# Optimization experiments

Hardware: AMD Instinct MI355X
Metric: run time of the kernel (lower is better)

Reference implementation:

```python
import jax, jax.numpy as jnp
import numpy as np

LAYER_SIZES = [1024, 1024, 1024, 1024, 1024, 1024, 512]
MAX_PATHS = 128
BATCH = 128
N_LAYERS = len(LAYER_SIZES) - 1


def setup_inputs() -> dict:
    key = jax.random.key(0)
    keys = jax.random.split(key, 1 + 2 * N_LAYERS)
    inp = {"x": jax.random.normal(keys[0], (BATCH, LAYER_SIZES[0]), dtype=jnp.float32)}
    for i in range(N_LAYERS):
        inp[f"W{i}"] = jax.random.normal(keys[1 + 2 * i], (LAYER_SIZES[i], LAYER_SIZES[i + 1]), dtype=jnp.float32) * 0.01
        inp[f"b{i}"] = jax.random.normal(keys[2 + 2 * i], (LAYER_SIZES[i + 1],), dtype=jnp.float32) * 0.01
    return inp


def _layer(data, W, b):
    # data: [B, in_feat, P] -> [B, out_feat, 3P]
    B, _, P = data.shape
    O = W.shape[1]
    pos = jnp.einsum('bfp,fo->bpo', data, W) + b          # [B, P, O]; neg branch is exactly -pos
    branches = jnp.stack([-pos, jnp.zeros_like(pos), pos], axis=-1)  # [B, P, O, 3]
    # transpose(1,2) then reshape: interleave branches per source path, matching torch
    return branches.transpose(0, 2, 1, 3).reshape(B, O, P * 3)


def _prune(data, keep):
    # keep top-`keep` paths by L2 norm over the feature dim
    norms = jnp.linalg.norm(data, axis=1)                 # [B, P]
    _, idx = jax.lax.top_k(norms, keep)                   # [B, keep]
    return jnp.take_along_axis(data, idx[:, None, :], axis=-1)


def _forward(x, Ws, bs):
    data = x[:, :, None]                                   # [B, F, 1]
    for i in range(N_LAYERS):
        data = _layer(data, Ws[i], bs[i])
        if i < N_LAYERS - 1:
            data = jnp.tanh(data)
        if data.shape[-1] > MAX_PATHS:
            data = _prune(data, MAX_PATHS)
    # collapse with 'max_abs': per (batch, feature) pick path with largest |value|
    idx = jnp.argmax(jnp.abs(data), axis=-1, keepdims=True)
    output = jnp.take_along_axis(data, idx, axis=-1).squeeze(-1)
    return output, data


def reference(x, W0, b0, W1, b1, W2, b2, W3, b3, W4, b4, W5, b5):
    Ws = [W0, W1, W2, W3, W4, W5]
    bs = [b0, b1, b2, b3, b4, b5]
    return _forward(x, Ws, bs)
```

## Files before the change

kernel.cpp:

```cpp
#include <hip/hip_runtime.h>
#include <math.h>


using s8v = __attribute__((ext_vector_type(8))) short;
using f4v = __attribute__((ext_vector_type(4))) float;

__device__ __forceinline__ float bf2f(short b) {
  unsigned u = ((unsigned)(unsigned short)b) << 16;
  return __builtin_bit_cast(float, u);
}
__device__ __forceinline__ short f2bf(float f) {
  unsigned u = __builtin_bit_cast(unsigned, f);
  u = (u + 0x7FFFu + ((u >> 16) & 1u)) >> 16;
  return (short)u;
}

struct TWArgs {
  const float* W[6];
  short* Th[6];
  short* Tl[6];
  const float* x;
  short* A0h;
  short* A0l;
  float* zone;
};
__global__ void __launch_bounds__(256)
transW_all(TWArgs a) {
  const int z = blockIdx.z;
  const int t = threadIdx.x;
  if (z == 6) {
    int bid = blockIdx.y * 16 + blockIdx.x;
    if (bid < 128) {
      int i = (bid * 256 + t) * 4;
      float4 v = *(const float4*)&a.x[i];
      short4 h, l;
      h.x = f2bf(v.x); l.x = f2bf(v.x - bf2f(h.x));
      h.y = f2bf(v.y); l.y = f2bf(v.y - bf2f(h.y));
      h.z = f2bf(v.z); l.z = f2bf(v.z - bf2f(h.z));
      h.w = f2bf(v.w); l.w = f2bf(v.w - bf2f(h.w));
      *(short4*)&a.A0h[i] = h;
      *(short4*)&a.A0l[i] = l;
    } else if (bid < 176) {
      a.zone[(bid - 128) * 256 + t] = 0.f;
    }
    return;
  }
  const int N = (z == 5) ? 512 : 1024;
  const int n0 = blockIdx.x * 64, k0 = blockIdx.y * 64;
  if (n0 >= N) return;
  const float* __restrict__ W = a.W[z];
  short* __restrict__ Th = a.Th[z];
  short* __restrict__ Tl = a.Tl[z];
  __shared__ float tile[64][65];
  const int r = t >> 4, c4 = (t & 15) * 4;
#pragma unroll
  for (int i = 0; i < 4; ++i) {
    int rr = r + 16 * i;
    float4 v = *(const float4*)&W[(size_t)(k0 + rr) * N + n0 + c4];
    tile[rr][c4 + 0] = v.x;
    tile[rr][c4 + 1] = v.y;
    tile[rr][c4 + 2] = v.z;
    tile[rr][c4 + 3] = v.w;
  }
  __syncthreads();
#pragma unroll
  for (int i = 0; i < 4; ++i) {
    int n = r + 16 * i;
    short4 h, l;
    float f0 = tile[c4 + 0][n], f1 = tile[c4 + 1][n];
    float f2 = tile[c4 + 2][n], f3 = tile[c4 + 3][n];
    h.x = f2bf(f0); l.x = f2bf(f0 - bf2f(h.x));
    h.y = f2bf(f1); l.y = f2bf(f1 - bf2f(h.y));
    h.z = f2bf(f2); l.z = f2bf(f2 - bf2f(h.z));
    h.w = f2bf(f3); l.w = f2bf(f3 - bf2f(h.w));
    size_t o = (size_t)(n0 + n) * 1024 + k0 + c4;
    *(short4*)&Th[o] = h;
    *(short4*)&Tl[o] = l;
  }
}

template <int EPI, int D, int KS>
__global__ void __launch_bounds__(256, 3)
mfma_gemm(const short* __restrict__ Ah, const short* __restrict__ Al,
          const short* __restrict__ Bh, const short* __restrict__ Bl,
          const float* __restrict__ bias, short* __restrict__ Oh,
          short* __restrict__ Ol, float* __restrict__ Of,
          float* __restrict__ ns, float* __restrict__ dotv,
          float* __restrict__ nrmv, int N, int Dn) {
  constexpr int KC = 1024 / KS;
  constexpr int BKP = 40;
  __shared__ short As_h[64 * BKP], As_l[64 * BKP];
  __shared__ short Bs_h[64 * BKP], Bs_l[64 * BKP];
  __shared__ float et[64][68];
  const int t = threadIdx.x;
  const int row0 = blockIdx.y * 64;
  const int col0 = blockIdx.x * 64;
  const int kb = blockIdx.z * KC;
  const int sr = t >> 2, sko = (t & 3) * 8;
  const short* Ahp = Ah + (size_t)(row0 + sr) * 1024 + kb + sko;
  const short* Alp = Al + (size_t)(row0 + sr) * 1024 + kb + sko;
  const short* Bhp = Bh + (size_t)(col0 + sr) * 1024 + kb + sko;
  const short* Blp = Bl + (size_t)(col0 + sr) * 1024 + kb + sko;
  const int w = t >> 6, lane = t & 63;
  const int l16 = lane & 15, q = lane >> 4;
  const int wm0 = (w & 1) * 32, wn0 = (w >> 1) * 32;
  const int abase = (wm0 + l16) * BKP + q * 8;
  const int bbase = (wn0 + l16) * BKP + q * 8;
  f4v acc[2][2];
#pragma unroll
  for (int i = 0; i < 2; ++i)
#pragma unroll
    for (int j = 0; j < 2; ++j) acc[i][j] = (f4v){0.f, 0.f, 0.f, 0.f};
  uint4 rah = *(const uint4*)(Ahp);
  uint4 ral = *(const uint4*)(Alp);
  uint4 rbh = *(const uint4*)(Bhp);
  uint4 rbl = *(const uint4*)(Blp);
  for (int k0 = 0; k0 < KC; k0 += 32) {
    __syncthreads();
    *(uint4*)&As_h[sr * BKP + sko] = rah;
    *(uint4*)&As_l[sr * BKP + sko] = ral;
    *(uint4*)&Bs_h[sr * BKP + sko] = rbh;
    *(uint4*)&Bs_l[sr * BKP + sko] = rbl;
    if (k0 + 32 < KC) {
      rah = *(const uint4*)(Ahp + k0 + 32);
      ral = *(const uint4*)(Alp + k0 + 32);
      rbh = *(const uint4*)(Bhp + k0 + 32);
      rbl = *(const uint4*)(Blp + k0 + 32);
    }
    __syncthreads();
    s8v ah[2], al[2], bh[2], bl[2];
#pragma unroll
    for (int mt = 0; mt < 2; ++mt) {
      ah[mt] = *(const s8v*)&As_h[abase + mt * 16 * BKP];
      al[mt] = *(const s8v*)&As_l[abase + mt * 16 * BKP];
    }
#pragma unroll
    for (int nt = 0; nt < 2; ++nt) {
      bh[nt] = *(const s8v*)&Bs_h[bbase + nt * 16 * BKP];
      bl[nt] = *(const s8v*)&Bs_l[bbase + nt * 16 * BKP];
    }
#pragma unroll
    for (int mt = 0; mt < 2; ++mt)
#pragma unroll
      for (int nt = 0; nt < 2; ++nt) {
        acc[mt][nt] = __builtin_amdgcn_mfma_f32_16x16x32_bf16(
            ah[mt], bh[nt], acc[mt][nt], 0, 0, 0);
        acc[mt][nt] = __builtin_amdgcn_mfma_f32_16x16x32_bf16(
            ah[mt], bl[nt], acc[mt][nt], 0, 0, 0);
        acc[mt][nt] = __builtin_amdgcn_mfma_f32_16x16x32_bf16(
            al[mt], bh[nt], acc[mt][nt], 0, 0, 0);
      }
  }

#pragma unroll
  for (int mt = 0; mt < 2; ++mt)
#pragma unroll
    for (int nt = 0; nt < 2; ++nt)
#pragma unroll
      for (int r = 0; r < 4; ++r)
        et[wm0 + mt * 16 + q * 4 + r][wn0 + nt * 16 + l16] = acc[mt][nt][r];
  __syncthreads();
  const int rl = t >> 2, cc = (t & 3) * 16;
  float v[16];
#pragma unroll
  for (int j = 0; j < 16; ++j) v[j] = et[rl][cc + j];
  const int rr = row0 + rl;

  if constexpr (EPI == 0) {
    const int R = (int)gridDim.y << 6;
    float* dst = Of + ((size_t)blockIdx.z * R + rr) * N + col0 + cc;
#pragma unroll
    for (int i = 0; i < 4; ++i)
      *(float4*)&dst[4 * i] =
          make_float4(v[4 * i], v[4 * i + 1], v[4 * i + 2], v[4 * i + 3]);
  } else if constexpr (EPI == 1) {
    const int b = rr / D, u = rr - b * D;
    const size_t ob = (size_t)(b * Dn) * (size_t)N + col0 + cc;
    const size_t om = ob + (size_t)(1 + 2 * u) * N;
    const size_t op = ob + (size_t)(2 + 2 * u) * N;
    uint mh[8], ml[8], ph[8], pl[8];
    float sm = 0.f, sp = 0.f;
#pragma unroll
    for (int j2 = 0; j2 < 8; ++j2) {
      float bc0 = bias[col0 + cc + 2 * j2];
      float bc1 = bias[col0 + cc + 2 * j2 + 1];
      float tm0 = tanhf(bc0 - v[2 * j2]), tm1 = tanhf(bc1 - v[2 * j2 + 1]);
      float tp0 = tanhf(bc0 + v[2 * j2]), tp1 = tanhf(bc1 + v[2 * j2 + 1]);
      short h0 = f2bf(tm0), h1 = f2bf(tm1);
      short g0 = f2bf(tm0 - bf2f(h0)), g1 = f2bf(tm1 - bf2f(h1));
      mh[j2] = (uint)(unsigned short)h0 | ((uint)(unsigned short)h1 << 16);
      ml[j2] = (uint)(unsigned short)g0 | ((uint)(unsigned short)g1 << 16);
      h0 = f2bf(tp0); h1 = f2bf(tp1);
      g0 = f2bf(tp0 - bf2f(h0)); g1 = f2bf(tp1 - bf2f(h1));
      ph[j2] = (uint)(unsigned short)h0 | ((uint)(unsigned short)h1 << 16);
      pl[j2] = (uint)(unsigned short)g0 | ((uint)(unsigned short)g1 << 16);
      sm = fmaf(tm0, tm0, fmaf(tm1, tm1, sm));
      sp = fmaf(tp0, tp0, fmaf(tp1, tp1, sp));
    }
    *(uint4*)&Oh[om] = make_uint4(mh[0], mh[1], mh[2], mh[3]);
    *(uint4*)&Oh[om + 8] = make_uint4(mh[4], mh[5], mh[6], mh[7]);
    *(uint4*)&Ol[om] = make_uint4(ml[0], ml[1], ml[2], ml[3]);
    *(uint4*)&Ol[om + 8] = make_uint4(ml[4], ml[5], ml[6], ml[7]);
    *(uint4*)&Oh[op] = make_uint4(ph[0], ph[1], ph[2], ph[3]);
    *(uint4*)&Oh[op + 8] = make_uint4(ph[4], ph[5], ph[6], ph[7]);
    *(uint4*)&Ol[op] = make_uint4(pl[0], pl[1], pl[2], pl[3]);
    *(uint4*)&Ol[op + 8] = make_uint4(pl[4], pl[5], pl[6], pl[7]);
    sm += __shfl_xor(sm, 1); sm += __shfl_xor(sm, 2);
    sp += __shfl_xor(sp, 1); sp += __shfl_xor(sp, 2);
    if ((t & 3) == 0) {
      atomicAdd(&ns[b * Dn + 1 + 2 * u], sm);
      atomicAdd(&ns[b * Dn + 2 + 2 * u], sp);
    }
    if (u == 0) {
      uint zh[8], zl[8];
      float sz = 0.f;
#pragma unroll
      for (int j2 = 0; j2 < 8; ++j2) {
        float tz0 = tanhf(bias[col0 + cc + 2 * j2]);
        float tz1 = tanhf(bias[col0 + cc + 2 * j2 + 1]);
        short h0 = f2bf(tz0), h1 = f2bf(tz1);
        short g0 = f2bf(tz0 - bf2f(h0)), g1 = f2bf(tz1 - bf2f(h1));
        zh[j2] = (uint)(unsigned short)h0 | ((uint)(unsigned short)h1 << 16);
        zl[j2] = (uint)(unsigned short)g0 | ((uint)(unsigned short)g1 << 16);
        sz = fmaf(tz0, tz0, fmaf(tz1, tz1, sz));
      }
      *(uint4*)&Oh[ob] = make_uint4(zh[0], zh[1], zh[2], zh[3]);
      *(uint4*)&Oh[ob + 8] = make_uint4(zh[4], zh[5], zh[6], zh[7]);
      *(uint4*)&Ol[ob] = make_uint4(zl[0], zl[1], zl[2], zl[3]);
      *(uint4*)&Ol[ob + 8] = make_uint4(zl[4], zl[5], zl[6], zl[7]);
      sz += __shfl_xor(sz, 1); sz += __shfl_xor(sz, 2);
      if ((t & 3) == 0) atomicAdd(&ns[b * Dn], sz);
    }
  } else {
    float nr = 0.f, dt = 0.f;
    float* dst = Of + (size_t)rr * N + col0 + cc;
#pragma unroll
    for (int j = 0; j < 16; ++j) {
      nr = fmaf(v[j], v[j], nr);
      dt = fmaf(v[j], bias[col0 + cc + j], dt);
    }
#pragma unroll
    for (int i = 0; i < 4; ++i)
      *(float4*)&dst[4 * i] =
          make_float4(v[4 * i], v[4 * i + 1], v[4 * i + 2], v[4 * i + 3]);
    nr += __shfl_xor(nr, 1); nr += __shfl_xor(nr, 2);
    dt += __shfl_xor(dt, 1); dt += __shfl_xor(dt, 2);
    if ((t & 3) == 0) {
      atomicAdd(&nrmv[rr], nr);
      atomicAdd(&dotv[rr], dt);
    }
  }
}

template <int KS>
__global__ void __launch_bounds__(256)
comb0_hl(const float* __restrict__ P, const float* __restrict__ bias,
         short* __restrict__ Oh, short* __restrict__ Ol, int R, int N) {
  int i = blockIdx.x * 256 + threadIdx.x;
  int n4 = N >> 2;
  int r = i / n4, c4 = (i - r * n4) * 4;
  float4 y = *(const float4*)&P[(size_t)r * N + c4];
  size_t stride = (size_t)R * N;
#pragma unroll
  for (int ks = 1; ks < KS; ++ks) {
    const float4 p = *(const float4*)&P[ks * stride + (size_t)r * N + c4];
    y.x += p.x; y.y += p.y; y.z += p.z; y.w += p.w;
  }
  float4 bc = *(const float4*)(bias + c4);
  float t0 = tanhf(bc.x + y.x), t1 = tanhf(bc.y + y.y);
  float t2 = tanhf(bc.z + y.z), t3 = tanhf(bc.w + y.w);
  short4 h, l;
  h.x = f2bf(t0); l.x = f2bf(t0 - bf2f(h.x));
  h.y = f2bf(t1); l.y = f2bf(t1 - bf2f(h.y));
  h.z = f2bf(t2); l.z = f2bf(t2 - bf2f(h.z));
  h.w = f2bf(t3); l.w = f2bf(t3 - bf2f(h.w));
  *(short4*)&Oh[(size_t)r * N + c4] = h;
  *(short4*)&Ol[(size_t)r * N + c4] = l;
}

template <int KS, int D>
__global__ void __launch_bounds__(256)
comb1_hl(const float* __restrict__ P, const float* __restrict__ bias,
         short* __restrict__ Oh, short* __restrict__ Ol, int R, int N,
         int Dn) {
  int i = blockIdx.x * 256 + threadIdx.x;
  int n4 = N >> 2;
  int r = i / n4, c4 = (i - r * n4) * 4;
  int b = r / D, u = r - b * D;
  float4 y = *(const float4*)&P[(size_t)r * N + c4];
  size_t stride = (size_t)R * N;
#pragma unroll
  for (int ks = 1; ks < KS; ++ks) {
    const float4 p = *(const float4*)&P[ks * stride + (size_t)r * N + c4];
    y.x += p.x; y.y += p.y; y.z += p.z; y.w += p.w;
  }
  float4 bc = *(const float4*)(bias + c4);
  size_t ob = (size_t)(b * Dn) * N + c4;
  size_t om = ob + (size_t)(1 + 2 * u) * N;
  size_t op = ob + (size_t)(2 + 2 * u) * N;
  {
    float t0 = tanhf(bc.x - y.x), t1 = tanhf(bc.y - y.y);
    float t2 = tanhf(bc.z - y.z), t3 = tanhf(bc.w - y.w);
    short4 h, l;
    h.x = f2bf(t0); l.x = f2bf(t0 - bf2f(h.x));
    h.y = f2bf(t1); l.y = f2bf(t1 - bf2f(h.y));
    h.z = f2bf(t2); l.z = f2bf(t2 - bf2f(h.z));
    h.w = f2bf(t3); l.w = f2bf(t3 - bf2f(h.w));
    *(short4*)&Oh[om] = h;
    *(short4*)&Ol[om] = l;
  }
  {
    float t0 = tanhf(bc.x + y.x), t1 = tanhf(bc.y + y.y);
    float t2 = tanhf(bc.z + y.z), t3 = tanhf(bc.w + y.w);
    short4 h, l;
    h.x = f2bf(t0); l.x = f2bf(t0 - bf2f(h.x));
    h.y = f2bf(t1); l.y = f2bf(t1 - bf2f(h.y));
    h.z = f2bf(t2); l.z = f2bf(t2 - bf2f(h.z));
    h.w = f2bf(t3); l.w = f2bf(t3 - bf2f(h.w));
    *(short4*)&Oh[op] = h;
    *(short4*)&Ol[op] = l;
  }
  if (u == 0) {
    float t0 = tanhf(bc.x), t1 = tanhf(bc.y);
    float t2 = tanhf(bc.z), t3 = tanhf(bc.w);
    short4 h, l;
    h.x = f2bf(t0); l.x = f2bf(t0 - bf2f(h.x));
    h.y = f2bf(t1); l.y = f2bf(t1 - bf2f(h.y));
    h.z = f2bf(t2); l.z = f2bf(t2 - bf2f(h.z));
    h.w = f2bf(t3); l.w = f2bf(t3 - bf2f(h.w));
    *(short4*)&Oh[ob] = h;
    *(short4*)&Ol[ob] = l;
  }
}

__global__ void __launch_bounds__(256)
prune4_k(const float* __restrict__ ns, int* __restrict__ kept4) {
  int b = blockIdx.x, t = threadIdx.x;
  __shared__ float nss[31];
  __shared__ float key[243];
  __shared__ int cls[243];
  if (t < 31) nss[t] = ns[b * 31 + t];
  __syncthreads();
  if (t < 243) {
    int j = t / 3, t4 = t - 3 * j;
    int d0 = j / 27, d1 = (j / 9) % 3, d2 = (j / 3) % 3, d3 = j % 3;
    int u = 0;
    u = (d0 == 1) ? 0 : (1 + 2 * u + (d0 == 2));
    u = (d1 == 1) ? 0 : (1 + 2 * u + (d1 == 2));
    u = (d2 == 1) ? 0 : (1 + 2 * u + (d2 == 2));
    u = (d3 == 1) ? 0 : (1 + 2 * u + (d3 == 2));
    cls[t] = u;
    key[t] = (t4 == 1) ? 0.f : nss[u];
  }
  __syncthreads();
  if (t < 243) {
    float k = key[t];
    int rank = 0;
    for (int e = 0; e < 243; ++e) {
      float ke = key[e];
      rank += (ke > k) || (ke == k && e < t);
    }
    if (rank < 128) {
      int t4 = t - 3 * (t / 3);
      kept4[b * 128 + rank] = (cls[t] << 1) | (t4 == 2 ? 1 : 0);
    }
  }
}

__global__ void __launch_bounds__(384)
prune5_k(const float* __restrict__ dotv, const float* __restrict__ nrmv,
         const float* __restrict__ b5, const int* __restrict__ kept4,
         int* __restrict__ kept5) {
  int b = blockIdx.x, t = threadIdx.x;
  __shared__ float red[384];
  __shared__ float pns[128];
  __shared__ float key[384];
  float p = 0.f;
  for (int o = t; o < 512; o += 384) p = fmaf(b5[o], b5[o], p);
  red[t] = p;
  __syncthreads();
  if (t < 128) red[t] = red[t] + red[t + 128] + red[t + 256];
  __syncthreads();
  if (t < 64) red[t] += red[t + 64];
  __syncthreads();
  if (t < 32) red[t] += red[t + 32];
  __syncthreads();
  if (t < 16) red[t] += red[t + 16];
  __syncthreads();
  if (t < 8) red[t] += red[t + 8];
  __syncthreads();
  if (t < 4) red[t] += red[t + 4];
  __syncthreads();
  if (t < 2) red[t] += red[t + 2];
  __syncthreads();
  if (t == 0) red[0] += red[1];
  __syncthreads();
  float nb5 = red[0];
  if (t < 128) {
    int k4 = kept4[b * 128 + t];
    int c = k4 >> 1;
    float s = (k4 & 1) ? 1.f : -1.f;
    pns[t] = nb5 + nrmv[b * 31 + c] + s * 2.f * dotv[b * 31 + c];
  }
  __syncthreads();
  int m = t / 3, tt = t - 3 * m;
  key[t] = (tt == 1) ? 0.f : pns[m];
  __syncthreads();
  float k = key[t];
  int rank = 0;
  for (int e = 0; e < 384; ++e) {
    float ke = key[e];
    rank += (ke > k) || (ke == k && e < t);
  }
  if (rank < 128) kept5[b * 128 + rank] = (m << 1) | (tt == 2 ? 1 : 0);
}

__global__ void __launch_bounds__(256)
finalize_k(const float* __restrict__ Y5, const float* __restrict__ b5,
           const int* __restrict__ kept4, const int* __restrict__ kept5,
           float* __restrict__ out, float* __restrict__ dataout) {
  const int b = blockIdx.y;
  const int o0 = blockIdx.x * 64;
  __shared__ float Ys[31][65];
  __shared__ float bias_s[64];
  __shared__ float vt[64][130];
  __shared__ float ra[64][4];
  __shared__ float rv[64][4];
  const int t = threadIdx.x;
  for (int idx = t; idx < 31 * 64; idx += 256) {
    int c = idx >> 6, o = idx & 63;
    Ys[c][o] = Y5[((size_t)b * 31 + c) * 512 + o0 + o];
  }
  if (t < 64) bias_s[t] = b5[o0 + t];
  const int rr = t & 127, oh = t >> 7;
  int k5 = kept5[b * 128 + rr];
  int m = k5 >> 1;
  float sig = (k5 & 1) ? 1.f : -1.f;
  int k4 = kept4[b * 128 + m];
  int cc = k4 >> 1;
  float s4 = (k4 & 1) ? 1.f : -1.f;
  float afac = sig * s4;
  __syncthreads();
#pragma unroll
  for (int ol = 0; ol < 32; ++ol) {
    int o = oh * 32 + ol;
    float v = sig * bias_s[o] + afac * Ys[cc][o];
    dataout[((size_t)b * 512 + o0 + o) * 128 + rr] = v;
    vt[o][rr] = v;
  }
  __syncthreads();
  int o = t >> 2, q = t & 3;
  float bestv = vt[o][q * 32];
  float besta = fabsf(bestv);
  for (int i = 1; i < 32; ++i) {
    float v = vt[o][q * 32 + i];
    float a = fabsf(v);
    if (a > besta) {
      besta = a;
      bestv = v;
    }
  }
  ra[o][q] = besta;
  rv[o][q] = bestv;
  __syncthreads();
  if (t < 64) {
    float ba = ra[t][0], bv = rv[t][0];
#pragma unroll
    for (int qq = 1; qq < 4; ++qq) {
      if (ra[t][qq] > ba) {
        ba = ra[t][qq];
        bv = rv[t][qq];
      }
    }
    out[(size_t)b * 512 + o0 + t] = bv;
  }
}

extern "C" void kernel_launch(void* const* d_in, const int* in_sizes, int n_in,
                              void* d_out, int out_size, void* d_ws,
                              size_t ws_size, hipStream_t stream) {
  const float* x = (const float*)d_in[0];
  const float* Wt[6];
  const float* bs[6];
  for (int i = 0; i < 6; ++i) {
    Wt[i] = (const float*)d_in[1 + 2 * i];
    bs[i] = (const float*)d_in[2 + 2 * i];
  }
  char* base = (char*)d_ws;
  short* A0h = (short*)(base + 0);
  short* A0l = (short*)(base + 262144);
  short* Wh[6], *Wl[6];
  {
    size_t off = 524288;
    for (int i = 0; i < 6; ++i) {
      size_t sz = (i < 5) ? 2097152 : 1048576;
      Wh[i] = (short*)(base + off);
      Wl[i] = (short*)(base + off + sz);
      off += 2 * sz;
    }
  }
  short* C1h = (short*)(base + 23592960), *C1l = (short*)(base + 23855104);
  short* C2h = (short*)(base + 24117248), *C2l = (short*)(base + 24903680);
  short* C3h = (short*)(base + 25690112), *C3l = (short*)(base + 27525120);
  short* C4h = (short*)(base + 29360128), *C4l = (short*)(base + 33292288);
  short* C5h = (short*)(base + 524288);
  short* C5l = (short*)(base + 8912896);
  float* PA = (float*)(base + 29360128);
  float* PB = (float*)(base + 524288);
  float* Y5 = (float*)(base + 23592960);
  float* ns = (float*)(base + 37224448);
  float* dotv = ns + 3968;
  float* nrmv = dotv + 3968;
  int* kept4 = (int*)(base + 37273600);
  int* kept5 = (int*)(base + 37339136);
  float* outp = (float*)d_out;
  float* dataout = outp + 128 * 512;

  dim3 blk(256);
  TWArgs twa;
  for (int i = 0; i < 6; ++i) {
    twa.W[i] = Wt[i];
    twa.Th[i] = Wh[i];
    twa.Tl[i] = Wl[i];
  }
  twa.x = x;
  twa.A0h = A0h;
  twa.A0l = A0l;
  twa.zone = ns;
  transW_all<<<dim3(16, 16, 7), blk, 0, stream>>>(twa);

  mfma_gemm<0, 1, 8><<<dim3(16, 2, 8), blk, 0, stream>>>(
      A0h, A0l, Wh[0], Wl[0], nullptr, nullptr, nullptr, PA, nullptr, nullptr,
      nullptr, 1024, 1);
  comb0_hl<8><<<dim3(128), blk, 0, stream>>>(PA, bs[0], C1h, C1l, 128, 1024);
  mfma_gemm<0, 1, 8><<<dim3(16, 2, 8), blk, 0, stream>>>(
      C1h, C1l, Wh[1], Wl[1], nullptr, nullptr, nullptr, PA, nullptr, nullptr,
      nullptr, 1024, 3);
  comb1_hl<8, 1><<<dim3(128), blk, 0, stream>>>(PA, bs[1], C2h, C2l, 128, 1024,
                                                3);
  mfma_gemm<0, 3, 4><<<dim3(16, 6, 4), blk, 0, stream>>>(
      C2h, C2l, Wh[2], Wl[2], nullptr, nullptr, nullptr, PA, nullptr, nullptr,
      nullptr, 1024, 7);
  comb1_hl<4, 3><<<dim3(384), blk, 0, stream>>>(PA, bs[2], C3h, C3l, 384, 1024,
                                                7);
  mfma_gemm<0, 7, 2><<<dim3(16, 14, 2), blk, 0, stream>>>(
      C3h, C3l, Wh[3], Wl[3], nullptr, nullptr, nullptr, PB, nullptr, nullptr,
      nullptr, 1024, 15);
  comb1_hl<2, 7><<<dim3(896), blk, 0, stream>>>(PB, bs[3], C4h, C4l, 896, 1024,
                                                15);
  mfma_gemm<1, 15, 1><<<dim3(16, 30), blk, 0, stream>>>(
      C4h, C4l, Wh[4], Wl[4], bs[4], C5h, C5l, nullptr, ns, nullptr, nullptr,
      1024, 31);
  prune4_k<<<dim3(128), blk, 0, stream>>>(ns, kept4);
  mfma_gemm<2, 31, 1><<<dim3(8, 62), blk, 0, stream>>>(
      C5h, C5l, Wh[5], Wl[5], bs[5], nullptr, nullptr, Y5, nullptr, dotv, nrmv,
      512, 0);
  prune5_k<<<dim3(128), dim3(384), 0, stream>>>(dotv, nrmv, bs[5], kept4,
                                                kept5);
  finalize_k<<<dim3(8, 128), blk, 0, stream>>>(Y5, bs[5], kept4, kept5, outp,
                                               dataout);
}
```

Measured before the change: 242.5 us.

## Add 128x128-tile GEMM variant for the three largest layers

Splits the GEMM into a small-tile variant (64x64, store only) for the early layers and a new 128x128-tile variant with 4x4 MFMA fragments per wave for layers 3-5. The big tile doubles register and LDS reuse of the A/B fragments, stages bias in shared memory, and reuses the tile LDS for a two-pass epilogue. The layer-3 split-K factor changes from 2 to 4. Workspace buffers are relocated so the bigger outputs no longer alias the weight buffers. The trade-off is fewer blocks per layer (e.g. 120 and 124 for layers 4 and 5), lower occupancy (launch bound 2), and higher register pressure.

After: 393.5 us. 62.3% more time.

```diff
diff --git a/kernel.cpp b/kernel.cpp
--- a/kernel.cpp
+++ b/kernel.cpp
@@ -79,14 +79,11 @@
   }
 }
 
-template <int EPI, int D, int KS>
+template <int KS>
 __global__ void __launch_bounds__(256, 3)
-mfma_gemm(const short* __restrict__ Ah, const short* __restrict__ Al,
-          const short* __restrict__ Bh, const short* __restrict__ Bl,
-          const float* __restrict__ bias, short* __restrict__ Oh,
-          short* __restrict__ Ol, float* __restrict__ Of,
-          float* __restrict__ ns, float* __restrict__ dotv,
-          float* __restrict__ nrmv, int N, int Dn) {
+mfma_gemm_s(const short* __restrict__ Ah, const short* __restrict__ Al,
+            const short* __restrict__ Bh, const short* __restrict__ Bl,
+            float* __restrict__ Of, int N) {
   constexpr int KC = 1024 / KS;
   constexpr int BKP = 40;
   __shared__ short As_h[64 * BKP], As_l[64 * BKP];
@@ -151,7 +148,6 @@
             al[mt], bh[nt], acc[mt][nt], 0, 0, 0);
       }
   }
-
 #pragma unroll
   for (int mt = 0; mt < 2; ++mt)
 #pragma unroll
@@ -165,89 +161,211 @@
 #pragma unroll
   for (int j = 0; j < 16; ++j) v[j] = et[rl][cc + j];
   const int rr = row0 + rl;
-
-  if constexpr (EPI == 0) {
-    const int R = (int)gridDim.y << 6;
-    float* dst = Of + ((size_t)blockIdx.z * R + rr) * N + col0 + cc;
-#pragma unroll
-    for (int i = 0; i < 4; ++i)
-      *(float4*)&dst[4 * i] =
-          make_float4(v[4 * i], v[4 * i + 1], v[4 * i + 2], v[4 * i + 3]);
-  } else if constexpr (EPI == 1) {
-    const int b = rr / D, u = rr - b * D;
-    const size_t ob = (size_t)(b * Dn) * (size_t)N + col0 + cc;
-    const size_t om = ob + (size_t)(1 + 2 * u) * N;
-    const size_t op = ob + (size_t)(2 + 2 * u) * N;
-    uint mh[8], ml[8], ph[8], pl[8];
-    float sm = 0.f, sp = 0.f;
-#pragma unroll
-    for (int j2 = 0; j2 < 8; ++j2) {
-      float bc0 = bias[col0 + cc + 2 * j2];
-      float bc1 = bias[col0 + cc + 2 * j2 + 1];
-      float tm0 = tanhf(bc0 - v[2 * j2]), tm1 = tanhf(bc1 - v[2 * j2 + 1]);
-      float tp0 = tanhf(bc0 + v[2 * j2]), tp1 = tanhf(bc1 + v[2 * j2 + 1]);
-      short h0 = f2bf(tm0), h1 = f2bf(tm1);
-      short g0 = f2bf(tm0 - bf2f(h0)), g1 = f2bf(tm1 - bf2f(h1));
-      mh[j2] = (uint)(unsigned short)h0 | ((uint)(unsigned short)h1 << 16);
-      ml[j2] = (uint)(unsigned short)g0 | ((uint)(unsigned short)g1 << 16);
-      h0 = f2bf(tp0); h1 = f2bf(tp1);
-      g0 = f2bf(tp0 - bf2f(h0)); g1 = f2bf(tp1 - bf2f(h1));
-      ph[j2] = (uint)(unsigned short)h0 | ((uint)(unsigned short)h1 << 16);
-      pl[j2] = (uint)(unsigned short)g0 | ((uint)(unsigned short)g1 << 16);
-      sm = fmaf(tm0, tm0, fmaf(tm1, tm1, sm));
-      sp = fmaf(tp0, tp0, fmaf(tp1, tp1, sp));
-    }
-    *(uint4*)&Oh[om] = make_uint4(mh[0], mh[1], mh[2], mh[3]);
-    *(uint4*)&Oh[om + 8] = make_uint4(mh[4], mh[5], mh[6], mh[7]);
-    *(uint4*)&Ol[om] = make_uint4(ml[0], ml[1], ml[2], ml[3]);
-    *(uint4*)&Ol[om + 8] = make_uint4(ml[4], ml[5], ml[6], ml[7]);
-    *(uint4*)&Oh[op] = make_uint4(ph[0], ph[1], ph[2], ph[3]);
-    *(uint4*)&Oh[op + 8] = make_uint4(ph[4], ph[5], ph[6], ph[7]);
-    *(uint4*)&Ol[op] = make_uint4(pl[0], pl[1], pl[2], pl[3]);
-    *(uint4*)&Ol[op + 8] = make_uint4(pl[4], pl[5], pl[6], pl[7]);
-    sm += __shfl_xor(sm, 1); sm += __shfl_xor(sm, 2);
-    sp += __shfl_xor(sp, 1); sp += __shfl_xor(sp, 2);
-    if ((t & 3) == 0) {
-      atomicAdd(&ns[b * Dn + 1 + 2 * u], sm);
-      atomicAdd(&ns[b * Dn + 2 + 2 * u], sp);
-    }
-    if (u == 0) {
-      uint zh[8], zl[8];
-      float sz = 0.f;
-#pragma unroll
-      for (int j2 = 0; j2 < 8; ++j2) {
-        float tz0 = tanhf(bias[col0 + cc + 2 * j2]);
-        float tz1 = tanhf(bias[col0 + cc + 2 * j2 + 1]);
-        short h0 = f2bf(tz0), h1 = f2bf(tz1);
-        short g0 = f2bf(tz0 - bf2f(h0)), g1 = f2bf(tz1 - bf2f(h1));
-        zh[j2] = (uint)(unsigned short)h0 | ((uint)(unsigned short)h1 << 16);
-        zl[j2] = (uint)(unsigned short)g0 | ((uint)(unsigned short)g1 << 16);
-        sz = fmaf(tz0, tz0, fmaf(tz1, tz1, sz));
-      }
-      *(uint4*)&Oh[ob] = make_uint4(zh[0], zh[1], zh[2], zh[3]);
-      *(uint4*)&Oh[ob + 8] = make_uint4(zh[4], zh[5], zh[6], zh[7]);
-      *(uint4*)&Ol[ob] = make_uint4(zl[0], zl[1], zl[2], zl[3]);
-      *(uint4*)&Ol[ob + 8] = make_uint4(zl[4], zl[5], zl[6], zl[7]);
-      sz += __shfl_xor(sz, 1); sz += __shfl_xor(sz, 2);
-      if ((t & 3) == 0) atomicAdd(&ns[b * Dn], sz);
-    }
-  } else {
-    float nr = 0.f, dt = 0.f;
-    float* dst = Of + (size_t)rr * N + col0 + cc;
-#pragma unroll
-    for (int j = 0; j < 16; ++j) {
-      nr = fmaf(v[j], v[j], nr);
-      dt = fmaf(v[j], bias[col0 + cc + j], dt);
-    }
-#pragma unroll
-    for (int i = 0; i < 4; ++i)
-      *(float4*)&dst[4 * i] =
-          make_float4(v[4 * i], v[4 * i + 1], v[4 * i + 2], v[4 * i + 3]);
-    nr += __shfl_xor(nr, 1); nr += __shfl_xor(nr, 2);
-    dt += __shfl_xor(dt, 1); dt += __shfl_xor(dt, 2);
-    if ((t & 3) == 0) {
-      atomicAdd(&nrmv[rr], nr);
-      atomicAdd(&dotv[rr], dt);
+  const int R = (int)gridDim.y << 6;
+  float* dst = Of + ((size_t)blockIdx.z * R + rr) * N + col0 + cc;
+#pragma unroll
+  for (int i = 0; i < 4; ++i)
+    *(float4*)&dst[4 * i] =
+        make_float4(v[4 * i], v[4 * i + 1], v[4 * i + 2], v[4 * i + 3]);
+}
+
+template <int EPI, int D, int KS>
+__global__ void __launch_bounds__(256, 2)
+mfma_gemm_b(const short* __restrict__ Ah, const short* __restrict__ Al,
+            const short* __restrict__ Bh, const short* __restrict__ Bl,
+            const float* __restrict__ bias, short* __restrict__ Oh,
+            short* __restrict__ Ol, float* __restrict__ Of,
+            float* __restrict__ ns, float* __restrict__ dotv,
+            float* __restrict__ nrmv, int N, int Dn) {
+  constexpr int KC = 1024 / KS;
+  constexpr int BKP = 40;
+  __shared__ short smem[4 * 128 * BKP];
+  short* As_h = smem;
+  short* As_l = smem + 128 * BKP;
+  short* Bs_h = smem + 2 * 128 * BKP;
+  short* Bs_l = smem + 3 * 128 * BKP;
+  float* et = (float*)smem;
+  __shared__ float bias_s[128];
+  const int t = threadIdx.x;
+  const int row0 = blockIdx.y * 128;
+  const int col0 = blockIdx.x * 128;
+  const int kb = blockIdx.z * KC;
+  if (EPI >= 1 && t < 32)
+    *(float4*)&bias_s[t * 4] = *(const float4*)&bias[col0 + t * 4];
+  const int sr = t >> 1, sko = (t & 1) * 16;
+  const short* Ahp = Ah + (size_t)(row0 + sr) * 1024 + kb + sko;
+  const short* Alp = Al + (size_t)(row0 + sr) * 1024 + kb + sko;
+  const short* Bhp = Bh + (size_t)(col0 + sr) * 1024 + kb + sko;
+  const short* Blp = Bl + (size_t)(col0 + sr) * 1024 + kb + sko;
+  const int w = t >> 6, lane = t & 63;
+  const int l16 = lane & 15, q = lane >> 4;
+  const int wm0 = (w & 1) * 64, wn0 = (w >> 1) * 64;
+  f4v acc[4][4];
+#pragma unroll
+  for (int i = 0; i < 4; ++i)
+#pragma unroll
+    for (int j = 0; j < 4; ++j) acc[i][j] = (f4v){0.f, 0.f, 0.f, 0.f};
+  uint4 rah[2], ral[2], rbh[2], rbl[2];
+#pragma unroll
+  for (int j = 0; j < 2; ++j) {
+    rah[j] = *(const uint4*)(Ahp + 8 * j);
+    ral[j] = *(const uint4*)(Alp + 8 * j);
+    rbh[j] = *(const uint4*)(Bhp + 8 * j);
+    rbl[j] = *(const uint4*)(Blp + 8 * j);
+  }
+  for (int k0 = 0; k0 < KC; k0 += 32) {
+    __syncthreads();
+#pragma unroll
+    for (int j = 0; j < 2; ++j) {
+      *(uint4*)&As_h[sr * BKP + sko + 8 * j] = rah[j];
+      *(uint4*)&As_l[sr * BKP + sko + 8 * j] = ral[j];
+      *(uint4*)&Bs_h[sr * BKP + sko + 8 * j] = rbh[j];
+      *(uint4*)&Bs_l[sr * BKP + sko + 8 * j] = rbl[j];
+    }
+    if (k0 + 32 < KC) {
+#pragma unroll
+      for (int j = 0; j < 2; ++j) {
+        rah[j] = *(const uint4*)(Ahp + k0 + 32 + 8 * j);
+        ral[j] = *(const uint4*)(Alp + k0 + 32 + 8 * j);
+        rbh[j] = *(const uint4*)(Bhp + k0 + 32 + 8 * j);
+        rbl[j] = *(const uint4*)(Blp + k0 + 32 + 8 * j);
+      }
+    }
+    __syncthreads();
+    s8v ah[4], al[4], bh[4], bl[4];
+#pragma unroll
+    for (int mt = 0; mt < 4; ++mt) {
+      int o = (wm0 + mt * 16 + l16) * BKP + q * 8;
+      ah[mt] = *(const s8v*)&As_h[o];
+      al[mt] = *(const s8v*)&As_l[o];
+    }
+#pragma unroll
+    for (int nt = 0; nt < 4; ++nt) {
+      int o = (wn0 + nt * 16 + l16) * BKP + q * 8;
+      bh[nt] = *(const s8v*)&Bs_h[o];
+      bl[nt] = *(const s8v*)&Bs_l[o];
+    }
+#pragma unroll
+    for (int mt = 0; mt < 4; ++mt)
+#pragma unroll
+      for (int nt = 0; nt < 4; ++nt) {
+        acc[mt][nt] = __builtin_amdgcn_mfma_f32_16x16x32_bf16(
+            ah[mt], bh[nt], acc[mt][nt], 0, 0, 0);
+        acc[mt][nt] = __builtin_amdgcn_mfma_f32_16x16x32_bf16(
+            ah[mt], bl[nt], acc[mt][nt], 0, 0, 0);
+        acc[mt][nt] = __builtin_amdgcn_mfma_f32_16x16x32_bf16(
+            al[mt], bh[nt], acc[mt][nt], 0, 0, 0);
+      }
+  }
+
+  const int rl = t >> 2, cc4 = (t & 3) * 32;
+  for (int pp = 0; pp < 2; ++pp) {
+    __syncthreads();
+    if ((w & 1) == pp) {
+#pragma unroll
+      for (int mt = 0; mt < 4; ++mt)
+#pragma unroll
+        for (int nt = 0; nt < 4; ++nt)
+#pragma unroll
+          for (int r = 0; r < 4; ++r)
+            et[(mt * 16 + q * 4 + r) * 132 + wn0 + nt * 16 + l16] =
+                acc[mt][nt][r];
+    }
+    __syncthreads();
+    float v[32];
+#pragma unroll
+    for (int j = 0; j < 32; ++j) v[j] = et[rl * 132 + cc4 + j];
+    const int rr = row0 + pp * 64 + rl;
+
+    if constexpr (EPI == 0) {
+      const int R = (int)gridDim.y << 7;
+      float* dst = Of + ((size_t)blockIdx.z * R + rr) * N + col0 + cc4;
+#pragma unroll
+      for (int i = 0; i < 8; ++i)
+        *(float4*)&dst[4 * i] =
+            make_float4(v[4 * i], v[4 * i + 1], v[4 * i + 2], v[4 * i + 3]);
+    } else if constexpr (EPI == 1) {
+      const int b = rr / D, u = rr - b * D;
+      const size_t ob = (size_t)(b * Dn) * (size_t)N + col0 + cc4;
+      const size_t om = ob + (size_t)(1 + 2 * u) * N;
+      const size_t op = ob + (size_t)(2 + 2 * u) * N;
+      uint mh[16], ml[16], qh[16], ql[16];
+      float sm = 0.f, sp = 0.f;
+#pragma unroll
+      for (int j2 = 0; j2 < 16; ++j2) {
+        float bc0 = bias_s[cc4 + 2 * j2];
+        float bc1 = bias_s[cc4 + 2 * j2 + 1];
+        float tm0 = tanhf(bc0 - v[2 * j2]), tm1 = tanhf(bc1 - v[2 * j2 + 1]);
+        float tp0 = tanhf(bc0 + v[2 * j2]), tp1 = tanhf(bc1 + v[2 * j2 + 1]);
+        short h0 = f2bf(tm0), h1 = f2bf(tm1);
+        short g0 = f2bf(tm0 - bf2f(h0)), g1 = f2bf(tm1 - bf2f(h1));
+        mh[j2] = (uint)(unsigned short)h0 | ((uint)(unsigned short)h1 << 16);
+        ml[j2] = (uint)(unsigned short)g0 | ((uint)(unsigned short)g1 << 16);
+        h0 = f2bf(tp0); h1 = f2bf(tp1);
+        g0 = f2bf(tp0 - bf2f(h0)); g1 = f2bf(tp1 - bf2f(h1));
+        qh[j2] = (uint)(unsigned short)h0 | ((uint)(unsigned short)h1 << 16);
+        ql[j2] = (uint)(unsigned short)g0 | ((uint)(unsigned short)g1 << 16);
+        sm = fmaf(tm0, tm0, fmaf(tm1, tm1, sm));
+        sp = fmaf(tp0, tp0, fmaf(tp1, tp1, sp));
+      }
+#pragma unroll
+      for (int i = 0; i < 4; ++i) {
+        *(uint4*)&Oh[om + 8 * i] =
+            make_uint4(mh[4 * i], mh[4 * i + 1], mh[4 * i + 2], mh[4 * i + 3]);
+        *(uint4*)&Ol[om + 8 * i] =
+            make_uint4(ml[4 * i], ml[4 * i + 1], ml[4 * i + 2], ml[4 * i + 3]);
+        *(uint4*)&Oh[op + 8 * i] =
+            make_uint4(qh[4 * i], qh[4 * i + 1], qh[4 * i + 2], qh[4 * i + 3]);
+        *(uint4*)&Ol[op + 8 * i] =
+            make_uint4(ql[4 * i], ql[4 * i + 1], ql[4 * i + 2], ql[4 * i + 3]);
+      }
+      sm += __shfl_xor(sm, 1); sm += __shfl_xor(sm, 2);
+      sp += __shfl_xor(sp, 1); sp += __shfl_xor(sp, 2);
+      if ((t & 3) == 0) {
+        atomicAdd(&ns[b * Dn + 1 + 2 * u], sm);
+        atomicAdd(&ns[b * Dn + 2 + 2 * u], sp);
+      }
+      if (u == 0) {
+        float sz = 0.f;
+        uint zh[16], zl[16];
+#pragma unroll
+        for (int j2 = 0; j2 < 16; ++j2) {
+          float tz0 = tanhf(bias_s[cc4 + 2 * j2]);
+          float tz1 = tanhf(bias_s[cc4 + 2 * j2 + 1]);
+          short h0 = f2bf(tz0), h1 = f2bf(tz1);
+          short g0 = f2bf(tz0 - bf2f(h0)), g1 = f2bf(tz1 - bf2f(h1));
+          zh[j2] = (uint)(unsigned short)h0 | ((uint)(unsigned short)h1 << 16);
+          zl[j2] = (uint)(unsigned short)g0 | ((uint)(unsigned short)g1 << 16);
+          sz = fmaf(tz0, tz0, fmaf(tz1, tz1, sz));
+        }
+#pragma unroll
+        for (int i = 0; i < 4; ++i) {
+          *(uint4*)&Oh[ob + 8 * i] = make_uint4(zh[4 * i], zh[4 * i + 1],
+                                                zh[4 * i + 2], zh[4 * i + 3]);
+          *(uint4*)&Ol[ob + 8 * i] = make_uint4(zl[4 * i], zl[4 * i + 1],
+                                                zl[4 * i + 2], zl[4 * i + 3]);
+        }
+        sz += __shfl_xor(sz, 1); sz += __shfl_xor(sz, 2);
+        if ((t & 3) == 0) atomicAdd(&ns[b * Dn], sz);
+      }
+    } else {
+      float nr = 0.f, dt = 0.f;
+      float* dst = Of + (size_t)rr * N + col0 + cc4;
+#pragma unroll
+      for (int j = 0; j < 32; ++j) {
+        nr = fmaf(v[j], v[j], nr);
+        dt = fmaf(v[j], bias_s[cc4 + j], dt);
+      }
+#pragma unroll
+      for (int i = 0; i < 8; ++i)
+        *(float4*)&dst[4 * i] =
+            make_float4(v[4 * i], v[4 * i + 1], v[4 * i + 2], v[4 * i + 3]);
+      nr += __shfl_xor(nr, 1); nr += __shfl_xor(nr, 2);
+      dt += __shfl_xor(dt, 1); dt += __shfl_xor(dt, 2);
+      if ((t & 3) == 0) {
+        atomicAdd(&nrmv[rr], nr);
+        atomicAdd(&dotv[rr], dt);
+      }
     }
   }
 }
@@ -503,16 +621,16 @@
   short* C2h = (short*)(base + 24117248), *C2l = (short*)(base + 24903680);
   short* C3h = (short*)(base + 25690112), *C3l = (short*)(base + 27525120);
   short* C4h = (short*)(base + 29360128), *C4l = (short*)(base + 33292288);
-  short* C5h = (short*)(base + 524288);
-  short* C5l = (short*)(base + 8912896);
-  float* PA = (float*)(base + 29360128);
-  float* PB = (float*)(base + 524288);
-  float* Y5 = (float*)(base + 23592960);
-  float* ns = (float*)(base + 37224448);
+  short* C5h = (short*)(base + 37224448);
+  short* C5l = (short*)(base + 45350912);
+  float* Y5 = (float*)(base + 53477376);
+  float* PA = (float*)(base + 61603840);
+  float* PB = (float*)(base + 67895296);
+  float* ns = (float*)(base + 82575360);
   float* dotv = ns + 3968;
   float* nrmv = dotv + 3968;
-  int* kept4 = (int*)(base + 37273600);
-  int* kept5 = (int*)(base + 37339136);
+  int* kept4 = (int*)(base + 82624512);
+  int* kept5 = (int*)(base + 82690048);
   float* outp = (float*)d_out;
   float* dataout = outp + 128 * 512;
 
@@ -529,30 +647,27 @@
   twa.zone = ns;
   transW_all<<<dim3(16, 16, 7), blk, 0, stream>>>(twa);
 
-  mfma_gemm<0, 1, 8><<<dim3(16, 2, 8), blk, 0, stream>>>(
-      A0h, A0l, Wh[0], Wl[0], nullptr, nullptr, nullptr, PA, nullptr, nullptr,
-      nullptr, 1024, 1);
+  mfma_gemm_s<8><<<dim3(16, 2, 8), blk, 0, stream>>>(A0h, A0l, Wh[0], Wl[0],
+                                                     PA, 1024);
   comb0_hl<8><<<dim3(128), blk, 0, stream>>>(PA, bs[0], C1h, C1l, 128, 1024);
-  mfma_gemm<0, 1, 8><<<dim3(16, 2, 8), blk, 0, stream>>>(
-      C1h, C1l, Wh[1], Wl[1], nullptr, nullptr, nullptr, PA, nullptr, nullptr,
-      nullptr, 1024, 3);
+  mfma_gemm_s<8><<<dim3(16, 2, 8), blk, 0, stream>>>(C1h, C1l, Wh[1], Wl[1],
+                                                     PA, 1024);
   comb1_hl<8, 1><<<dim3(128), blk, 0, stream>>>(PA, bs[1], C2h, C2l, 128, 1024,
                                                 3);
-  mfma_gemm<0, 3, 4><<<dim3(16, 6, 4), blk, 0, stream>>>(
-      C2h, C2l, Wh[2], Wl[2], nullptr, nullptr, nullptr, PA, nullptr, nullptr,
-      nullptr, 1024, 7);
+  mfma_gemm_s<4><<<dim3(16, 6, 4), blk, 0, stream>>>(C2h, C2l, Wh[2], Wl[2],
+                                                     PA, 1024);
   comb1_hl<4, 3><<<dim3(384), blk, 0, stream>>>(PA, bs[2], C3h, C3l, 384, 1024,
                                                 7);
-  mfma_gemm<0, 7, 2><<<dim3(16, 14, 2), blk, 0, stream>>>(
+  mfma_gemm_b<0, 7, 4><<<dim3(8, 7, 4), blk, 0, stream>>>(
       C3h, C3l, Wh[3], Wl[3], nullptr, nullptr, nullptr, PB, nullptr, nullptr,
       nullptr, 1024, 15);
-  comb1_hl<2, 7><<<dim3(896), blk, 0, stream>>>(PB, bs[3], C4h, C4l, 896, 1024,
+  comb1_hl<4, 7><<<dim3(896), blk, 0, stream>>>(PB, bs[3], C4h, C4l, 896, 1024,
                                                 15);
-  mfma_gemm<1, 15, 1><<<dim3(16, 30), blk, 0, stream>>>(
+  mfma_gemm_b<1, 15, 1><<<dim3(8, 15), blk, 0, stream>>>(
       C4h, C4l, Wh[4], Wl[4], bs[4], C5h, C5l, nullptr, ns, nullptr, nullptr,
       1024, 31);
   prune4_k<<<dim3(128), blk, 0, stream>>>(ns, kept4);
-  mfma_gemm<2, 31, 1><<<dim3(8, 62), blk, 0, stream>>>(
+  mfma_gemm_b<2, 31, 1><<<dim3(4, 31), blk, 0, stream>>>(
       C5h, C5l, Wh[5], Wl[5], bs[5], nullptr, nullptr, Y5, nullptr, dotv, nrmv,
       512, 0);
   prune5_k<<<dim3(128), dim3(384), 0, stream>>>(dotv, nrmv, bs[5], kept4,
```
